# Kernel optimization log

Hardware: AMD Instinct MI355X
Metric: run time of the kernel (lower is better)

Reference implementation:

```python
import jax, jax.numpy as jnp
import numpy as np

EPS = 1e-6


def _rms_norm(x, w):
    # RMSNorm over last dim in fp32, like Qwen3RMSNorm
    x32 = x.astype(jnp.float32)
    var = jnp.mean(x32 * x32, axis=-1, keepdims=True)
    return (x32 * jax.lax.rsqrt(var + EPS)).astype(x.dtype) * w


def _rotate_half(x):
    h = x.shape[-1] // 2
    return jnp.concatenate([-x[..., h:], x[..., :h]], axis=-1)


def setup_inputs() -> dict:
    key = jax.random.key(0)
    ks = jax.random.split(key, 8)
    B, S, HID = 1, 8192, 1024
    H, HKV, D = 16, 8, 128
    n_seg = 8
    hidden_states = jax.random.normal(ks[0], (B, S, HID), dtype=jnp.float32)
    cu_seqlens = jnp.arange(n_seg + 1, dtype=jnp.int32) * (S // n_seg)
    # multimodal RoPE tables: two position streams, each [B, S, D]
    inv_freq = 1.0 / (1e6 ** (jnp.arange(0, D, 2, dtype=jnp.float32) / D))
    pos = jnp.arange(S, dtype=jnp.float32)
    ang0 = pos[:, None] * inv_freq[None, :]            # [S, D/2]
    ang1 = (pos[:, None] * 0.5) * inv_freq[None, :]    # second stream
    def tab(a):
        return jnp.concatenate([a, a], axis=-1)[None]   # [1, S, D]
    cos = jnp.stack([tab(jnp.cos(ang0)), tab(jnp.cos(ang1))], axis=0)  # [2,1,S,D]
    sin = jnp.stack([tab(jnp.sin(ang0)), tab(jnp.sin(ang1))], axis=0)
    sd = 0.02
    Wq = jax.random.normal(ks[1], (H * D, HID), dtype=jnp.float32) * sd
    Wk = jax.random.normal(ks[2], (HKV * D, HID), dtype=jnp.float32) * sd
    Wv = jax.random.normal(ks[3], (HKV * D, HID), dtype=jnp.float32) * sd
    Wo = jax.random.normal(ks[4], (HID, H * D), dtype=jnp.float32) * sd
    q_norm_w = 1.0 + jax.random.normal(ks[5], (D,), dtype=jnp.float32) * sd
    k_norm_w = 1.0 + jax.random.normal(ks[6], (D,), dtype=jnp.float32) * sd
    return {"hidden_states": hidden_states, "cu_seqlens": cu_seqlens,
            "cos": cos, "sin": sin, "Wq": Wq, "Wk": Wk, "Wv": Wv, "Wo": Wo,
            "q_norm_w": q_norm_w, "k_norm_w": k_norm_w}


def reference(hidden_states, cu_seqlens, cos, sin, Wq, Wk, Wv, Wo, q_norm_w, k_norm_w):
    B, S, _ = hidden_states.shape
    D = q_norm_w.shape[0]
    H = Wq.shape[0] // D
    HKV = Wk.shape[0] // D
    groups = H // HKV
    n_seg = cu_seqlens.shape[0] - 1   # equal-length segments (static)
    L = S // n_seg
    scaling = D ** -0.5

    # projections -> [B, H(kv), S, D]
    q = (hidden_states @ Wq.T).reshape(B, S, H, D).transpose(0, 2, 1, 3)
    k = (hidden_states @ Wk.T).reshape(B, S, HKV, D).transpose(0, 2, 1, 3)
    v = (hidden_states @ Wv.T).reshape(B, S, HKV, D).transpose(0, 2, 1, 3)

    q = _rms_norm(q, q_norm_w)
    k = _rms_norm(k, k_norm_w)

    # multimodal RoPE: interleave the two streams across the two half-dims
    half = D // 2
    cos_e = jnp.concatenate([cos[0, ..., :half], cos[1, ..., half:]], axis=-1)[:, None]  # [B,1,S,D]
    sin_e = jnp.concatenate([sin[0, ..., :half], sin[1, ..., half:]], axis=-1)[:, None]
    q = q * cos_e + _rotate_half(q) * sin_e
    k = k * cos_e + _rotate_half(k) * sin_e

    # GQA: repeat kv heads
    k = jnp.repeat(k, groups, axis=1)
    v = jnp.repeat(v, groups, axis=1)

    # block-diagonal attention over cu_seqlens segments (equal-length -> reshape)
    qb = q.reshape(B, H, n_seg, L, D)
    kb = k.reshape(B, H, n_seg, L, D)
    vb = v.reshape(B, H, n_seg, L, D)
    scores = jnp.einsum('bhnld,bhnmd->bhnlm', qb, kb) * scaling
    probs = jax.nn.softmax(scores, axis=-1)
    ob = jnp.einsum('bhnlm,bhnmd->bhnld', probs, vb)
    out = ob.reshape(B, H, S, D).transpose(0, 2, 1, 3).reshape(B, S, H * D)
    return out @ Wo.T
```

## Files before the change

kernel.cpp:

```cpp
#include <hip/hip_runtime.h>

#define S_LEN 8192
#define HID   1024
#define NH    16
#define NKV   8
#define HD    128
#define LSEG  1024

typedef float  f4  __attribute__((ext_vector_type(4)));
typedef _Float16 h4 __attribute__((ext_vector_type(4)));
typedef _Float16 h8 __attribute__((ext_vector_type(8)));

__device__ __forceinline__ void gl_lds16(const void* g, void* l) {
  __builtin_amdgcn_global_load_lds((const __attribute__((address_space(1))) void*)g,
                                   (__attribute__((address_space(3))) void*)l, 16, 0, 0);
}

__device__ __forceinline__ h8 ld8u(const _Float16* p) {
  h4 a = *(const h4*)p;
  h4 b = *(const h4*)(p + 4);
  return __builtin_shufflevector(a, b, 0, 1, 2, 3, 4, 5, 6, 7);
}

template <int CTRL>
__device__ __forceinline__ float dppf(float v) {
  return __builtin_bit_cast(float,
      __builtin_amdgcn_mov_dpp(__builtin_bit_cast(int, v), CTRL, 0xF, 0xF, true));
}
__device__ __forceinline__ float red16_max(float x) {
  x = fmaxf(x, dppf<0xB1>(x));
  x = fmaxf(x, dppf<0x4E>(x));
  x = fmaxf(x, dppf<0x141>(x));
  x = fmaxf(x, dppf<0x140>(x));
  return x;
}
__device__ __forceinline__ float red16_sum(float x) {
  x += dppf<0xB1>(x);
  x += dppf<0x4E>(x);
  x += dppf<0x141>(x);
  x += dppf<0x140>(x);
  return x;
}

__global__ void convert_kernel(const float* __restrict__ hid, const float* __restrict__ wq,
                               const float* __restrict__ wk, const float* __restrict__ wv,
                               const float* __restrict__ wo,
                               _Float16* __restrict__ hid16, _Float16* __restrict__ wqkv,
                               _Float16* __restrict__ wo16) {
  const int total4 = 3670016;
  for (int i = blockIdx.x * blockDim.x + threadIdx.x; i < total4; i += gridDim.x * blockDim.x) {
    int i4 = i * 4;
    const float* src; _Float16* dst;
    if      (i4 <  8388608) { src = hid + i4;              dst = hid16 + i4; }
    else if (i4 < 10485760) { src = wq + (i4 -  8388608);  dst = wqkv + (i4 - 8388608); }
    else if (i4 < 11534336) { src = wk + (i4 - 10485760);  dst = wqkv + 2097152 + (i4 - 10485760); }
    else if (i4 < 12582912) { src = wv + (i4 - 11534336);  dst = wqkv + 3145728 + (i4 - 11534336); }
    else                    { src = wo + (i4 - 12582912);  dst = wo16 + (i4 - 12582912); }
    f4 x = *(const f4*)src;
    h4 y; y[0]=(_Float16)x[0]; y[1]=(_Float16)x[1]; y[2]=(_Float16)x[2]; y[3]=(_Float16)x[3];
    *(h4*)dst = y;
  }
}

template <int FUSED>
__global__ __launch_bounds__(256, 3)
void gemm_kernel(const _Float16* __restrict__ A, const _Float16* __restrict__ B,
                 float* __restrict__ Cout, int K, int N,
                 const float* __restrict__ cosp, const float* __restrict__ sinp,
                 const float* __restrict__ qnw, const float* __restrict__ knw,
                 _Float16* __restrict__ q16, _Float16* __restrict__ k16,
                 _Float16* __restrict__ v16T) {
  __shared__ __align__(16) char smem[32768];

  const int tid = threadIdx.x, w = tid >> 6, ln = tid & 63;
  const int l15 = ln & 15, l4 = ln >> 4;
  const int m0 = blockIdx.y * 128, n0 = blockIdx.x * 128;
  const int sg_row = ln >> 2, sg_cho = (ln & 3) * 8;

  f4 acc[2][8] = {};

  for (int k0 = 0; k0 < K; k0 += 64) {
    __syncthreads();
#pragma unroll
    for (int r = 0; r < 2; r++) {
      int ch = r * 4 + w;
#pragma unroll
      for (int u = 0; u < 2; u++) {
        gl_lds16(A + (size_t)(m0 + ch * 16 + sg_row) * K + k0 + u * 32 + sg_cho,
                 smem + u * 8192 + ch * 1024);
        gl_lds16(B + (size_t)(n0 + ch * 16 + sg_row) * K + k0 + u * 32 + sg_cho,
                 smem + 16384 + u * 8192 + ch * 1024);
      }
    }
    __syncthreads();
#pragma unroll
    for (int u = 0; u < 2; u++) {
      const _Float16* As = (const _Float16*)(smem + u * 8192);
      const _Float16* Bs = (const _Float16*)(smem + 16384 + u * 8192);
      h8 af[2], bf[8];
#pragma unroll
      for (int mt = 0; mt < 2; mt++) af[mt] = *(const h8*)(As + (w * 32 + mt * 16 + l15) * 32 + l4 * 8);
#pragma unroll
      for (int nt = 0; nt < 8; nt++) bf[nt] = *(const h8*)(Bs + (nt * 16 + l15) * 32 + l4 * 8);
#pragma unroll
      for (int mt = 0; mt < 2; mt++)
#pragma unroll
        for (int nt = 0; nt < 8; nt++)
          acc[mt][nt] = __builtin_amdgcn_mfma_f32_16x16x32_f16(af[mt], bf[nt], acc[mt][nt], 0, 0, 0);
    }
  }

  if (!FUSED) {
#pragma unroll
    for (int mt = 0; mt < 2; mt++)
#pragma unroll
      for (int rg = 0; rg < 4; rg++) {
        int row = m0 + w * 32 + mt * 16 + l4 * 4 + rg;
#pragma unroll
        for (int nt = 0; nt < 8; nt++)
          Cout[(size_t)row * N + n0 + nt * 16 + l15] = acc[mt][nt][rg];
      }
    return;
  } else {
    const int head = blockIdx.x;
    if (head < 24) {
      const float* nw = (head < 16) ? qnw : knw;
      const float hs = (head < 16) ? 0.12751734f : 1.0f;
      _Float16* base = (head < 16) ? q16 + (size_t)head * S_LEN * HD
                                   : k16 + (size_t)(head - 16) * S_LEN * HD;
      float nwv[8];
#pragma unroll
      for (int nt = 0; nt < 8; nt++) nwv[nt] = nw[nt * 16 + l15];
#pragma unroll
      for (int mt = 0; mt < 2; mt++)
#pragma unroll
        for (int rg = 0; rg < 4; rg++) {
          const int row = m0 + w * 32 + mt * 16 + l4 * 4 + rg;
          float ss = 0.f;
#pragma unroll
          for (int nt = 0; nt < 8; nt++) ss += acc[mt][nt][rg] * acc[mt][nt][rg];
          ss = red16_sum(ss);
          const float sc = rsqrtf(ss * 0.0078125f + 1e-6f);
#pragma unroll
          for (int nt = 0; nt < 8; nt++) {
            const int c = nt * 16 + l15;
            const int str = (nt >= 4) ? 1048576 : 0;
            float x  = acc[mt][nt][rg] * sc * nwv[nt];
            float xp = acc[mt][nt ^ 4][rg] * sc * nwv[nt ^ 4];
            float ce = cosp[str + row * HD + c];
            float se = sinp[str + row * HD + c];
            float rot = (nt >= 4) ? xp : -xp;
            base[(size_t)row * HD + c] = (_Float16)((x * ce + rot * se) * hs);
          }
        }
    } else {
      _Float16* vb = v16T + (size_t)(head - 24) * S_LEN * HD;
#pragma unroll
      for (int mt = 0; mt < 2; mt++)
#pragma unroll
        for (int nt = 0; nt < 8; nt++) {
          h4 hv;
#pragma unroll
          for (int rg = 0; rg < 4; rg++) hv[rg] = (_Float16)acc[mt][nt][rg];
          *(h4*)&vb[(size_t)(nt * 16 + l15) * S_LEN + m0 + w * 32 + mt * 16 + l4 * 4] = hv;
        }
    }
  }
}

__global__ __launch_bounds__(256, 2)
void attn_kernel(const _Float16* __restrict__ q16, const _Float16* __restrict__ k16,
                 const _Float16* __restrict__ vT, _Float16* __restrict__ ao16) {
  const int tq = blockIdx.x, g = blockIdx.y, h = blockIdx.z;
  const int hkv = h >> 1;
  const int tid = threadIdx.x, w = tid >> 6, ln = tid & 63;
  const int l15 = ln & 15, l4 = ln >> 4;

  __shared__ _Float16 Qs[128 * 132];
  __shared__ _Float16 KP[128 * 68];
  __shared__ _Float16 Vt[128 * 68];

  const _Float16* qsrc = q16 + ((size_t)h * S_LEN + g * LSEG + tq * 128) * HD;
#pragma unroll
  for (int i = 0; i < 8; i++) {
    int c = tid + 256 * i, row = c >> 4, o = c & 15;
    uint4 v = *(const uint4*)(qsrc + row * HD + o * 8);
    *(uint2*)&Qs[row * 132 + o * 8]     = make_uint2(v.x, v.y);
    *(uint2*)&Qs[row * 132 + o * 8 + 4] = make_uint2(v.z, v.w);
  }

  f4 O[2][8] = {};
  float mr[2][4], lr[2][4];
#pragma unroll
  for (int mt = 0; mt < 2; mt++)
#pragma unroll
    for (int rg = 0; rg < 4; rg++) { mr[mt][rg] = -1e30f; lr[mt][rg] = 0.f; }

  const size_t kbase = ((size_t)hkv * S_LEN + g * LSEG) * HD;
  const size_t vbase = (size_t)hkv * S_LEN * HD + (size_t)g * LSEG;

  const int krow = tid >> 4, ko = tid & 15;
  const int vd   = tid >> 3, vo = tid & 7;

  uint4 kr[4], vr[4];
#pragma unroll
  for (int i = 0; i < 4; i++) {
    kr[i] = *(const uint4*)(k16 + kbase + (size_t)(krow + 16 * i) * HD + ko * 8);
    vr[i] = *(const uint4*)(vT + vbase + (size_t)(vd + 32 * i) * S_LEN + vo * 8);
  }
#pragma unroll
  for (int i = 0; i < 4; i++) {
    int row = krow + 16 * i;
    *(uint2*)&KP[row * 132 + ko * 8]     = make_uint2(kr[i].x, kr[i].y);
    *(uint2*)&KP[row * 132 + ko * 8 + 4] = make_uint2(kr[i].z, kr[i].w);
    int d = vd + 32 * i;
    *(uint2*)&Vt[d * 68 + vo * 8]     = make_uint2(vr[i].x, vr[i].y);
    *(uint2*)&Vt[d * 68 + vo * 8 + 4] = make_uint2(vr[i].z, vr[i].w);
  }

  for (int j = 0; j < 16; j++) {
    __syncthreads();

    const int jn = (j + 1) & 15;
#pragma unroll
    for (int i = 0; i < 4; i++) {
      kr[i] = *(const uint4*)(k16 + kbase + (size_t)(jn * 64 + krow + 16 * i) * HD + ko * 8);
      vr[i] = *(const uint4*)(vT + vbase + (size_t)(vd + 32 * i) * S_LEN + jn * 64 + vo * 8);
    }

    f4 s[2][4] = {};
#pragma unroll
    for (int kk = 0; kk < 4; kk++) {
      h8 a0 = ld8u(Qs + (w * 32 + l15) * 132 + kk * 32 + l4 * 8);
      h8 a1 = ld8u(Qs + (w * 32 + 16 + l15) * 132 + kk * 32 + l4 * 8);
#pragma unroll
      for (int nt = 0; nt < 4; nt++) {
        h8 b = ld8u(KP + (nt * 16 + l15) * 132 + kk * 32 + l4 * 8);
        s[0][nt] = __builtin_amdgcn_mfma_f32_16x16x32_f16(a0, b, s[0][nt], 0, 0, 0);
        s[1][nt] = __builtin_amdgcn_mfma_f32_16x16x32_f16(a1, b, s[1][nt], 0, 0, 0);
      }
    }

    float al[2][4];
#pragma unroll
    for (int mt = 0; mt < 2; mt++)
#pragma unroll
      for (int rg = 0; rg < 4; rg++) {
        float mx = fmaxf(fmaxf(s[mt][0][rg], s[mt][1][rg]), fmaxf(s[mt][2][rg], s[mt][3][rg]));
        mx = red16_max(mx);
        float mnew = fmaxf(mr[mt][rg], mx);
        float alpha = exp2f(mr[mt][rg] - mnew);
        mr[mt][rg] = mnew;
        float rs = 0.f;
#pragma unroll
        for (int nt = 0; nt < 4; nt++) {
          float p = exp2f(s[mt][nt][rg] - mnew);
          s[mt][nt][rg] = p;
          rs += p;
        }
        rs = red16_sum(rs);
        lr[mt][rg] = lr[mt][rg] * alpha + rs;
        al[mt][rg] = alpha;
      }

    __syncthreads();
#pragma unroll
    for (int mt = 0; mt < 2; mt++)
#pragma unroll
      for (int nt = 0; nt < 4; nt++)
#pragma unroll
        for (int rg = 0; rg < 4; rg++)
          KP[(w * 32 + mt * 16 + l4 * 4 + rg) * 68 + nt * 16 + l15] = (_Float16)s[mt][nt][rg];
#pragma unroll
    for (int mt = 0; mt < 2; mt++)
#pragma unroll
      for (int d8 = 0; d8 < 8; d8++)
#pragma unroll
        for (int rg = 0; rg < 4; rg++) O[mt][d8][rg] *= al[mt][rg];
    __syncthreads();

#pragma unroll
    for (int kk = 0; kk < 2; kk++) {
      h8 a0 = ld8u(KP + (w * 32 + l15) * 68 + kk * 32 + l4 * 8);
      h8 a1 = ld8u(KP + (w * 32 + 16 + l15) * 68 + kk * 32 + l4 * 8);
#pragma unroll
      for (int d8 = 0; d8 < 8; d8++) {
        h8 b = ld8u(Vt + (d8 * 16 + l15) * 68 + kk * 32 + l4 * 8);
        O[0][d8] = __builtin_amdgcn_mfma_f32_16x16x32_f16(a0, b, O[0][d8], 0, 0, 0);
        O[1][d8] = __builtin_amdgcn_mfma_f32_16x16x32_f16(a1, b, O[1][d8], 0, 0, 0);
      }
    }

    __syncthreads();
#pragma unroll
    for (int i = 0; i < 4; i++) {
      int row = krow + 16 * i;
      *(uint2*)&KP[row * 132 + ko * 8]     = make_uint2(kr[i].x, kr[i].y);
      *(uint2*)&KP[row * 132 + ko * 8 + 4] = make_uint2(kr[i].z, kr[i].w);
      int d = vd + 32 * i;
      *(uint2*)&Vt[d * 68 + vo * 8]     = make_uint2(vr[i].x, vr[i].y);
      *(uint2*)&Vt[d * 68 + vo * 8 + 4] = make_uint2(vr[i].z, vr[i].w);
    }
  }

  const size_t obase = (size_t)(g * LSEG + tq * 128);
#pragma unroll
  for (int mt = 0; mt < 2; mt++)
#pragma unroll
    for (int rg = 0; rg < 4; rg++) {
      float inv = 1.f / lr[mt][rg];
#pragma unroll
      for (int d8 = 0; d8 < 8; d8++)
        ao16[(obase + w * 32 + mt * 16 + l4 * 4 + rg) * 2048 + h * HD + d8 * 16 + l15] =
            (_Float16)(O[mt][d8][rg] * inv);
    }
}

extern "C" void kernel_launch(void* const* d_in, const int* in_sizes, int n_in,
                              void* d_out, int out_size, void* d_ws, size_t ws_size,
                              hipStream_t stream) {
  const float* hid  = (const float*)d_in[0];
  const float* cosp = (const float*)d_in[2];
  const float* sinp = (const float*)d_in[3];
  const float* wq   = (const float*)d_in[4];
  const float* wk   = (const float*)d_in[5];
  const float* wv   = (const float*)d_in[6];
  const float* wo   = (const float*)d_in[7];
  const float* qnw  = (const float*)d_in[8];
  const float* knw  = (const float*)d_in[9];
  float* out = (float*)d_out;

  _Float16* hid16 = (_Float16*)d_ws;
  _Float16* wqkv  = hid16 + 8388608;
  _Float16* wo16  = wqkv + 4194304;
  _Float16* q16   = wo16 + 2097152;
  _Float16* k16   = q16 + 16777216;
  _Float16* v16T  = k16 + 8388608;
  _Float16* ao16  = v16T + 8388608;

  convert_kernel<<<dim3(1024), dim3(256), 0, stream>>>(hid, wq, wk, wv, wo, hid16, wqkv, wo16);
  gemm_kernel<1><<<dim3(32, 64), dim3(256), 0, stream>>>(hid16, wqkv, nullptr, 1024, 4096,
                                                         cosp, sinp, qnw, knw, q16, k16, v16T);
  attn_kernel<<<dim3(8, 8, 16), dim3(256), 0, stream>>>(q16, k16, v16T, ao16);
  gemm_kernel<0><<<dim3(8, 64), dim3(256), 0, stream>>>(ao16, wo16, out, 2048, 1024,
                                                        nullptr, nullptr, nullptr, nullptr,
                                                        nullptr, nullptr, nullptr);
}
```

Measured before the change: 412.7 us.

## Swizzle workgroups for XCD L2 locality and skip lazy softmax rescaling

Remaps GEMM and attention workgroup IDs so that blocks sharing operands (the same KV head and segment, or adjacent GEMM tiles) land on the same XCD, which improves L2 reuse on the multi-die MI355X. Attention now uses a 1D grid that is decoded into segment, kv head, query tile and head. The online softmax also skips the max update and the O/l rescaling unless some row's max grows by more than 8 (log2 units) over the running max. Deferring rescaling bounds exp2 values by 2^8, so fp16 P values stay representable, but it relies on a wave-wide any-vote to stay correct.

Measured after the change: 405.4 us. About the same (-1.8%).

```diff
diff --git a/kernel.cpp b/kernel.cpp
--- a/kernel.cpp
+++ b/kernel.cpp
@@ -72,9 +72,15 @@
                  _Float16* __restrict__ v16T) {
   __shared__ __align__(16) char smem[32768];
 
+  constexpr int GX  = FUSED ? 32 : 8;
+  constexpr int NWG = FUSED ? 2048 : 512;
+  const int lin = blockIdx.y * GX + blockIdx.x;
+  const int swz = (lin & 7) * (NWG >> 3) + (lin >> 3);
+  const int bx = swz & (GX - 1), by = swz / GX;
+
   const int tid = threadIdx.x, w = tid >> 6, ln = tid & 63;
   const int l15 = ln & 15, l4 = ln >> 4;
-  const int m0 = blockIdx.y * 128, n0 = blockIdx.x * 128;
+  const int m0 = by * 128, n0 = bx * 128;
   const int sg_row = ln >> 2, sg_cho = (ln & 3) * 8;
 
   f4 acc[2][8] = {};
@@ -122,7 +128,7 @@
       }
     return;
   } else {
-    const int head = blockIdx.x;
+    const int head = bx;
     if (head < 24) {
       const float* nw = (head < 16) ? qnw : knw;
       const float hs = (head < 16) ? 0.12751734f : 1.0f;
@@ -171,8 +177,13 @@
 __global__ __launch_bounds__(256, 2)
 void attn_kernel(const _Float16* __restrict__ q16, const _Float16* __restrict__ k16,
                  const _Float16* __restrict__ vT, _Float16* __restrict__ ao16) {
-  const int tq = blockIdx.x, g = blockIdx.y, h = blockIdx.z;
-  const int hkv = h >> 1;
+  const int bid = blockIdx.x;
+  const int xcd = bid & 7, slot = bid >> 3;
+  const int grp = xcd * 8 + (slot >> 4);
+  const int mem = slot & 15;
+  const int g = grp >> 3, hkv = grp & 7;
+  const int tq = mem & 7, h = hkv * 2 + (mem >> 3);
+
   const int tid = threadIdx.x, w = tid >> 6, ln = tid & 63;
   const int l15 = ln & 15, l4 = ln >> 4;
 
@@ -241,26 +252,43 @@
       }
     }
 
+    float mx[2][4];
+    bool nd = false;
+#pragma unroll
+    for (int mt = 0; mt < 2; mt++)
+#pragma unroll
+      for (int rg = 0; rg < 4; rg++) {
+        float m = fmaxf(fmaxf(s[mt][0][rg], s[mt][1][rg]), fmaxf(s[mt][2][rg], s[mt][3][rg]));
+        m = red16_max(m);
+        mx[mt][rg] = m;
+        nd = nd || (m > mr[mt][rg] + 8.f);
+      }
+    const bool needr = __any((int)nd) != 0;
     float al[2][4];
+    if (needr) {
+#pragma unroll
+      for (int mt = 0; mt < 2; mt++)
+#pragma unroll
+        for (int rg = 0; rg < 4; rg++) {
+          float mnew = fmaxf(mr[mt][rg], mx[mt][rg]);
+          al[mt][rg] = exp2f(mr[mt][rg] - mnew);
+          mr[mt][rg] = mnew;
+        }
+    }
 #pragma unroll
     for (int mt = 0; mt < 2; mt++)
 #pragma unroll
       for (int rg = 0; rg < 4; rg++) {
-        float mx = fmaxf(fmaxf(s[mt][0][rg], s[mt][1][rg]), fmaxf(s[mt][2][rg], s[mt][3][rg]));
-        mx = red16_max(mx);
-        float mnew = fmaxf(mr[mt][rg], mx);
-        float alpha = exp2f(mr[mt][rg] - mnew);
-        mr[mt][rg] = mnew;
         float rs = 0.f;
 #pragma unroll
         for (int nt = 0; nt < 4; nt++) {
-          float p = exp2f(s[mt][nt][rg] - mnew);
+          float p = exp2f(s[mt][nt][rg] - mr[mt][rg]);
           s[mt][nt][rg] = p;
           rs += p;
         }
         rs = red16_sum(rs);
-        lr[mt][rg] = lr[mt][rg] * alpha + rs;
-        al[mt][rg] = alpha;
+        if (needr) lr[mt][rg] = lr[mt][rg] * al[mt][rg] + rs;
+        else       lr[mt][rg] += rs;
       }
 
     __syncthreads();
@@ -271,12 +299,14 @@
 #pragma unroll
         for (int rg = 0; rg < 4; rg++)
           KP[(w * 32 + mt * 16 + l4 * 4 + rg) * 68 + nt * 16 + l15] = (_Float16)s[mt][nt][rg];
-#pragma unroll
-    for (int mt = 0; mt < 2; mt++)
-#pragma unroll
-      for (int d8 = 0; d8 < 8; d8++)
-#pragma unroll
-        for (int rg = 0; rg < 4; rg++) O[mt][d8][rg] *= al[mt][rg];
+    if (needr) {
+#pragma unroll
+      for (int mt = 0; mt < 2; mt++)
+#pragma unroll
+        for (int d8 = 0; d8 < 8; d8++)
+#pragma unroll
+          for (int rg = 0; rg < 4; rg++) O[mt][d8][rg] *= al[mt][rg];
+    }
     __syncthreads();
 
 #pragma unroll
@@ -341,7 +371,7 @@
   convert_kernel<<<dim3(1024), dim3(256), 0, stream>>>(hid, wq, wk, wv, wo, hid16, wqkv, wo16);
   gemm_kernel<1><<<dim3(32, 64), dim3(256), 0, stream>>>(hid16, wqkv, nullptr, 1024, 4096,
                                                          cosp, sinp, qnw, knw, q16, k16, v16T);
-  attn_kernel<<<dim3(8, 8, 16), dim3(256), 0, stream>>>(q16, k16, v16T, ao16);
+  attn_kernel<<<dim3(1024), dim3(256), 0, stream>>>(q16, k16, v16T, ao16);
   gemm_kernel<0><<<dim3(8, 64), dim3(256), 0, stream>>>(ao16, wo16, out, 2048, 1024,
                                                         nullptr, nullptr, nullptr, nullptr,
                                                         nullptr, nullptr, nullptr);
```
